# Optimization experiments

Hardware: AMD Instinct MI355X
Metric: run time of the kernel (lower is better)

Reference implementation:

```python
import jax, jax.numpy as jnp
import numpy as np

B, P, Q, D = 16, 4096, 1024, 256


def setup_inputs() -> dict:
    key = jax.random.key(0)
    k1, k2, k3, k4 = jax.random.split(key, 4)
    return {
        "passage_encodes": jax.random.normal(k1, (B, P, D), dtype=jnp.float32),
        "question_encodes": jax.random.normal(k2, (B, Q, D), dtype=jnp.float32),
        "w_attn": jax.random.normal(k3, (2 * D, 1), dtype=jnp.float32) * (1.0 / np.sqrt(2 * D)),
        "b_attn": jnp.zeros((1,), dtype=jnp.float32),
        "w_out": jax.random.normal(k4, (2 * D, 256), dtype=jnp.float32) * (1.0 / np.sqrt(2 * D)),
        "b_out": jnp.zeros((256,), dtype=jnp.float32),
    }


def reference(passage_encodes, question_encodes, w_attn, b_attn, w_out, b_out):
    # similarity matrix [B, P, Q]
    sim = jnp.einsum('bpd,bqd->bpq', passage_encodes, question_encodes)
    # context-to-question attention
    c2q = jax.nn.softmax(sim, axis=-1)                       # [B, P, Q]
    ctx2q = jnp.einsum('bpq,bqd->bpd', c2q, question_encodes)  # [B, P, D]
    # question-to-context attention (softmax over row-max)
    q2c = jax.nn.softmax(jnp.max(sim, axis=-1), axis=-1)     # [B, P]
    q2c_vec = jnp.einsum('bp,bpd->bd', q2c, passage_encodes)  # [B, D]
    tp = jnp.tanh(passage_encodes)
    concat = jnp.concatenate([
        tp * jnp.tanh(ctx2q),
        tp * jnp.tanh(q2c_vec)[:, None, :],  # broadcast instead of repeat
    ], axis=-1)                                              # [B, P, 2D]
    # attention reducer: linear -> softmax over sequence -> weighted sum
    w = jax.nn.softmax(jnp.einsum('bpc,co->bp', concat, w_attn) + b_attn[0], axis=1)
    reduced = jnp.einsum('bp,bpc->bc', w, concat)            # [B, 2D]
    return reduced @ w_out + b_out                            # [B, output_dim]
```

## Files before the change

kernel.cpp:

```cpp
#include <hip/hip_runtime.h>
#include <cmath>

#define BB 16
#define PP 4096
#define QQ 1024
#define DD 256

typedef __attribute__((ext_vector_type(8))) short short8;
typedef __attribute__((ext_vector_type(4))) float floatx4;
typedef __attribute__((ext_vector_type(4))) _Float16 half4;

static __device__ inline ushort bf16_rne(float x) {
  unsigned u = __float_as_uint(x);
  unsigned r = (u + 0x7fffu + ((u >> 16) & 1u)) >> 16;
  return (ushort)r;
}
static __device__ inline float bf16f(ushort h) { return __uint_as_float(((unsigned)h) << 16); }

static __device__ inline float ftanh(float x) {
  float e = __expf(2.0f * x);
  return 1.0f - 2.0f * __builtin_amdgcn_rcpf(e + 1.0f);
}

static __device__ inline void gl16(const void* g, void* l) {
  __builtin_amdgcn_global_load_lds(
      (const __attribute__((address_space(1))) unsigned int*)g,
      (__attribute__((address_space(3))) unsigned int*)l, 16, 0, 0);
}

__global__ __launch_bounds__(256) void kQprep(
    const float* __restrict__ ques, ushort* __restrict__ qb)
{
  const int b = blockIdx.y, qt = blockIdx.x;
  __shared__ float tile[32][260];
  const int tid = threadIdx.x;
  const float* src = ques + ((size_t)b * QQ + qt * 32) * DD;
  for (int i = tid; i < 32 * 64; i += 256) {
    int r = i >> 6, c = (i & 63) << 2;
    *(float4*)&tile[r][c] = *(const float4*)(src + r * DD + c);
  }
  ushort* blob = qb + (size_t)(b * 32 + qt) * 24576;
  {
    int r = tid >> 3;
    int j0 = (tid & 7) * 4;
    const float* rowp = src + r * DD + j0 * 8;
    float xs[32];
#pragma unroll
    for (int q4 = 0; q4 < 8; ++q4)
      *(float4*)&xs[q4 * 4] = *(const float4*)(rowp + q4 * 4);
#pragma unroll
    for (int jj = 0; jj < 4; ++jj) {
      int j = j0 + jj;
      ushort h8[8], l8[8];
#pragma unroll
      for (int e = 0; e < 8; ++e) {
        float x = xs[jj * 8 + e];
        ushort h = bf16_rne(x);
        h8[e] = h; l8[e] = bf16_rne(x - bf16f(h));
      }
      int g = r * 32 + (j ^ (r & 7));
      *(uint4*)&blob[(size_t)g * 8] = *(uint4*)h8;
      *(uint4*)&blob[8192 + (size_t)g * 8] = *(uint4*)l8;
    }
  }
  __syncthreads();
  {
    int d = tid;
    int s = (d >> 1) & 3;
    ushort h32[32];
#pragma unroll
    for (int r = 0; r < 32; ++r) h32[r] = bf16_rne(tile[r][d]);
#pragma unroll
    for (int k = 0; k < 4; ++k) {
      ushort g8[8];
#pragma unroll
      for (int e = 0; e < 4; ++e) {
        g8[e]     = h32[k * 4 + e];
        g8[4 + e] = h32[16 + k * 4 + e];
      }
      *(uint4*)&blob[16384 + (size_t)d * 32 + (k ^ s) * 8] = *(uint4*)g8;
    }
  }
}

__global__ __launch_bounds__(512, 1) void kA(
    const float* __restrict__ pass, const ushort* __restrict__ qb,
    const float* __restrict__ w_attn,
    _Float16* __restrict__ first_h, _Float16* __restrict__ tp_h,
    float* __restrict__ logit1,
    float* __restrict__ numpart, float* __restrict__ denpart)
{
  __shared__ alignas(16) char sm[147456];

  const int b    = blockIdx.y;
  const int p0   = blockIdx.x * 128;
  const int tid  = threadIdx.x;
  const int w    = tid >> 6;
  const int lane = tid & 63;
  const int l15  = lane & 15;
  const int quad = lane >> 4;
  const int swz  = l15 & 7;

  short8 bhi[8], blo[8];
  {
    const float* prow = pass + (((size_t)b * PP + p0 + w * 16 + l15) * DD);
#pragma unroll
    for (int c = 0; c < 8; ++c) {
      const float* p8 = prow + c * 32 + quad * 8;
      float4 x0 = *(const float4*)p8;
      float4 x1 = *(const float4*)(p8 + 4);
      float xs[8] = {x0.x, x0.y, x0.z, x0.w, x1.x, x1.y, x1.z, x1.w};
#pragma unroll
      for (int j = 0; j < 8; ++j) {
        ushort h = bf16_rne(xs[j]);
        ushort lo = bf16_rne(xs[j] - bf16f(h));
        bhi[c][j] = (short)h;
        blo[c][j] = (short)lo;
      }
    }
  }

  int goff[8];
#pragma unroll
  for (int c = 0; c < 8; ++c) goff[c] = (l15 * 32 + ((4 * c + quad) ^ swz)) * 8;
  const int vtoff = l15 * 32 + ((quad ^ ((l15 >> 1) & 3)) * 8);

  const ushort* tb = qb + (size_t)b * 32 * 24576;
  const int dma_l = w * 3072 + lane * 8;
  const int dma_s = w * 6144 + lane * 16;

  floatx4 accO[16];
#pragma unroll
  for (int i = 0; i < 16; ++i) accO[i] = (floatx4){0.f, 0.f, 0.f, 0.f};
  float mx = -INFINITY, ps = 0.f;
  short8 phi = {0, 0, 0, 0, 0, 0, 0, 0}, plo = {0, 0, 0, 0, 0, 0, 0, 0};

  {
    const ushort* gs = tb + dma_l;
    char* ld = sm + dma_s;
#pragma unroll
    for (int i = 0; i < 6; ++i) gl16(gs + i * 512, ld + i * 1024);
  }
  __syncthreads();

  for (int t = 0; t < 32; ++t) {
    const int ic = t % 3, ip = (t + 2) % 3, inx = (t + 1) % 3;
    char* cur = sm + ic * 49152;
    char* prv = sm + ip * 49152;
    if (t < 31) {
      const ushort* gs = tb + (size_t)(t + 1) * 24576 + dma_l;
      char* ld = sm + inx * 49152 + dma_s;
#pragma unroll
      for (int i = 0; i < 6; ++i) gl16(gs + i * 512, ld + i * 1024);
    }

    const ushort* Qhi = (const ushort*)cur;
    const ushort* Qlo = (const ushort*)(cur + 16384);
    floatx4 s0 = (floatx4){0.f, 0.f, 0.f, 0.f};
    floatx4 s1 = (floatx4){0.f, 0.f, 0.f, 0.f};
#pragma unroll
    for (int c = 0; c < 8; ++c) {
      short8 a0h = *(const short8*)&Qhi[goff[c]];
      short8 a0l = *(const short8*)&Qlo[goff[c]];
      short8 a1h = *(const short8*)&Qhi[goff[c] + 4096];
      short8 a1l = *(const short8*)&Qlo[goff[c] + 4096];
      s0 = __builtin_amdgcn_mfma_f32_16x16x32_bf16(a0h, bhi[c], s0, 0, 0, 0);
      s0 = __builtin_amdgcn_mfma_f32_16x16x32_bf16(a0h, blo[c], s0, 0, 0, 0);
      s0 = __builtin_amdgcn_mfma_f32_16x16x32_bf16(a0l, bhi[c], s0, 0, 0, 0);
      s1 = __builtin_amdgcn_mfma_f32_16x16x32_bf16(a1h, bhi[c], s1, 0, 0, 0);
      s1 = __builtin_amdgcn_mfma_f32_16x16x32_bf16(a1h, blo[c], s1, 0, 0, 0);
      s1 = __builtin_amdgcn_mfma_f32_16x16x32_bf16(a1l, bhi[c], s1, 0, 0, 0);
    }

    if (t > 0) {
      const ushort* TQ = (const ushort*)(prv + 32768);
#pragma unroll
      for (int nt = 0; nt < 16; ++nt) {
        short8 vhi = *(const short8*)&TQ[nt * 512 + vtoff];
        accO[nt] = __builtin_amdgcn_mfma_f32_16x16x32_bf16(phi, vhi, accO[nt], 0, 0, 0);
        accO[nt] = __builtin_amdgcn_mfma_f32_16x16x32_bf16(plo, vhi, accO[nt], 0, 0, 0);
      }
    }

    {
      short8 nph, npl;
#pragma unroll
      for (int r = 0; r < 4; ++r) {
        float s = s0[r];
        mx = fmaxf(mx, s);
        float x = __expf(s - 60.f);
        ps += x;
        ushort h = bf16_rne(x);
        nph[r] = (short)h;
        npl[r] = (short)bf16_rne(x - bf16f(h));
      }
#pragma unroll
      for (int r = 0; r < 4; ++r) {
        float s = s1[r];
        mx = fmaxf(mx, s);
        float x = __expf(s - 60.f);
        ps += x;
        ushort h = bf16_rne(x);
        nph[4 + r] = (short)h;
        npl[4 + r] = (short)bf16_rne(x - bf16f(h));
      }
      phi = nph;
      plo = npl;
    }
    __syncthreads();
  }

  {
    const ushort* TQ = (const ushort*)(sm + 49152 + 32768);
#pragma unroll
    for (int nt = 0; nt < 16; ++nt) {
      short8 vhi = *(const short8*)&TQ[nt * 512 + vtoff];
      accO[nt] = __builtin_amdgcn_mfma_f32_16x16x32_bf16(phi, vhi, accO[nt], 0, 0, 0);
      accO[nt] = __builtin_amdgcn_mfma_f32_16x16x32_bf16(plo, vhi, accO[nt], 0, 0, 0);
    }
  }

  ps += __shfl_xor(ps, 16);
  ps += __shfl_xor(ps, 32);
  mx = fmaxf(mx, __shfl_xor(mx, 16));
  mx = fmaxf(mx, __shfl_xor(mx, 32));

  __syncthreads();
  float* Of = (float*)(sm + w * 16640);
#pragma unroll
  for (int nt = 0; nt < 16; ++nt)
#pragma unroll
    for (int r = 0; r < 4; ++r)
      Of[(quad * 4 + r) * 260 + nt * 16 + l15] = accO[nt][r];
  const float4 w1 = *(const float4*)(w_attn + lane * 4);
  const size_t rowoff = (size_t)b * PP + p0 + w * 16;
  float4 qacc = make_float4(0.f, 0.f, 0.f, 0.f);
  float dacc = 0.f;
#pragma unroll
  for (int j = 0; j < 16; ++j) {
    float4 o = *(const float4*)&Of[j * 260 + lane * 4];
    float linv = 1.f / __shfl(ps, j);
    float4 pv4 = *(const float4*)(pass + (rowoff + j) * DD + lane * 4);
    float wj = __expf(__shfl(mx, j) - 60.f);
    qacc.x += wj * pv4.x; qacc.y += wj * pv4.y;
    qacc.z += wj * pv4.z; qacc.w += wj * pv4.w;
    dacc += wj;
    float tpx = ftanh(pv4.x), tpy = ftanh(pv4.y), tpz = ftanh(pv4.z), tpw = ftanh(pv4.w);
    float4 f;
    f.x = tpx * ftanh(o.x * linv);
    f.y = tpy * ftanh(o.y * linv);
    f.z = tpz * ftanh(o.z * linv);
    f.w = tpw * ftanh(o.w * linv);
    half4 fh = {(_Float16)f.x, (_Float16)f.y, (_Float16)f.z, (_Float16)f.w};
    half4 th = {(_Float16)tpx, (_Float16)tpy, (_Float16)tpz, (_Float16)tpw};
    *(half4*)(first_h + (rowoff + j) * DD + lane * 4) = fh;
    *(half4*)(tp_h + (rowoff + j) * DD + lane * 4) = th;
    float part = f.x * w1.x + f.y * w1.y + f.z * w1.z + f.w * w1.w;
    part += __shfl_xor(part, 1);  part += __shfl_xor(part, 2);
    part += __shfl_xor(part, 4);  part += __shfl_xor(part, 8);
    part += __shfl_xor(part, 16); part += __shfl_xor(part, 32);
    if (lane == 0) logit1[rowoff + j] = part;
  }

  float* redw = (float*)(sm + w * 16640);
  *(float4*)&redw[lane * 4] = qacc;
  if (lane == 0) redw[256] = dacc;
  __syncthreads();
  if (w == 0) {
    float4 s = make_float4(0.f, 0.f, 0.f, 0.f);
    float dsum = 0.f;
#pragma unroll
    for (int wv = 0; wv < 8; ++wv) {
      const float* rp = (const float*)(sm + wv * 16640);
      float4 v = *(const float4*)&rp[lane * 4];
      s.x += v.x; s.y += v.y; s.z += v.z; s.w += v.w;
      dsum += rp[256];
    }
    *(float4*)(numpart + (size_t)(blockIdx.x * 16 + b) * DD + lane * 4) = s;
    if (lane == 0) denpart[blockIdx.x * 16 + b] = dsum;
  }
}

__global__ __launch_bounds__(256) void kE(
    const _Float16* __restrict__ tp_h, const _Float16* __restrict__ first_h,
    const float* __restrict__ logit1,
    const float* __restrict__ numpart, const float* __restrict__ denpart,
    const float* __restrict__ w_attn,
    float* __restrict__ r1part, float* __restrict__ r2part, float* __restrict__ den2part)
{
  const int b = blockIdx.y, chunk = blockIdx.x;
  const int tid = threadIdx.x, r = tid >> 6, ln = tid & 63;
  __shared__ float s1[4][64][4];
  __shared__ float s2[4][64][4];
  __shared__ float sd[4][64];
  __shared__ alignas(16) float w2s[256];
  {
    float num = 0.f, den = 0.f;
#pragma unroll
    for (int c = 0; c < 32; ++c) {
      num += numpart[(size_t)(c * 16 + b) * DD + tid];
      den += denpart[c * 16 + b];
    }
    w2s[tid] = w_attn[DD + tid] * ftanh(num / den);
  }
  __syncthreads();
  const float4 wv = *(const float4*)&w2s[ln << 2];
  const float* lg = logit1 + (size_t)b * PP + chunk * 64;
  const size_t base = ((size_t)b * PP + chunk * 64) * DD;
  float a1[4] = {0.f, 0.f, 0.f, 0.f}, a2[4] = {0.f, 0.f, 0.f, 0.f};
  float den = 0.f;
  for (int p = r; p < 64; p += 4) {
    half4 f = *(const half4*)(first_h + base + (size_t)p * DD + ln * 4);
    half4 t = *(const half4*)(tp_h + base + (size_t)p * DD + ln * 4);
    float part = (float)t.x * wv.x + (float)t.y * wv.y +
                 (float)t.z * wv.z + (float)t.w * wv.w;
    part += __shfl_xor(part, 1);  part += __shfl_xor(part, 2);
    part += __shfl_xor(part, 4);  part += __shfl_xor(part, 8);
    part += __shfl_xor(part, 16); part += __shfl_xor(part, 32);
    float wgt = __expf(lg[p] + part);
    a1[0] += wgt * (float)f.x; a1[1] += wgt * (float)f.y;
    a1[2] += wgt * (float)f.z; a1[3] += wgt * (float)f.w;
    a2[0] += wgt * (float)t.x; a2[1] += wgt * (float)t.y;
    a2[2] += wgt * (float)t.z; a2[3] += wgt * (float)t.w;
    den += wgt;
  }
  *(float4*)&s1[r][ln][0] = *(float4*)a1;
  *(float4*)&s2[r][ln][0] = *(float4*)a2;
  sd[r][ln] = den;
  __syncthreads();
  if (r == 0) {
    float o1[4], o2[4];
#pragma unroll
    for (int i = 0; i < 4; ++i) {
      o1[i] = s1[0][ln][i] + s1[1][ln][i] + s1[2][ln][i] + s1[3][ln][i];
      o2[i] = s2[0][ln][i] + s2[1][ln][i] + s2[2][ln][i] + s2[3][ln][i];
    }
    *(float4*)(r1part + (size_t)(chunk * 16 + b) * DD + ln * 4) = *(float4*)o1;
    *(float4*)(r2part + (size_t)(chunk * 16 + b) * DD + ln * 4) = *(float4*)o2;
    if (ln == 0)
      den2part[chunk * 16 + b] = sd[0][0] + sd[1][0] + sd[2][0] + sd[3][0];
  }
}

__global__ __launch_bounds__(256) void kF(
    const float* __restrict__ r1part, const float* __restrict__ r2part,
    const float* __restrict__ den2part,
    const float* __restrict__ numpart, const float* __restrict__ denpart,
    const float* __restrict__ w_out, const float* __restrict__ b_out,
    float* __restrict__ out)
{
  const int b = blockIdx.x >> 2, og = blockIdx.x & 3;
  const int tid = threadIdx.x;
  __shared__ alignas(16) float R1[256], R2[256];
  __shared__ float sacc[4][64];
  {
    float red1 = 0.f, red2 = 0.f, den2 = 0.f;
#pragma unroll
    for (int c = 0; c < 64; ++c) {
      red1 += r1part[(size_t)(c * 16 + b) * DD + tid];
      red2 += r2part[(size_t)(c * 16 + b) * DD + tid];
      den2 += den2part[c * 16 + b];
    }
    float num = 0.f, den = 0.f;
#pragma unroll
    for (int c = 0; c < 32; ++c) {
      num += numpart[(size_t)(c * 16 + b) * DD + tid];
      den += denpart[c * 16 + b];
    }
    float t = ftanh(num / den);
    float inv = 1.f / den2;
    R1[tid] = red1 * inv;
    R2[tid] = red2 * inv * t;
  }
  __syncthreads();
  const int oi = tid & 63, ks = tid >> 6;
  const int o = og * 64 + oi;
  float acc = 0.f;
  for (int k = ks * 64; k < ks * 64 + 64; ++k) {
    acc += R1[k] * w_out[k * 256 + o];
    acc += R2[k] * w_out[(DD + k) * 256 + o];
  }
  sacc[ks][oi] = acc;
  __syncthreads();
  if (ks == 0) {
    float v = sacc[0][oi] + sacc[1][oi] + sacc[2][oi] + sacc[3][oi];
    out[b * 256 + o] = v + b_out[o];
  }
}

extern "C" void kernel_launch(void* const* d_in, const int* in_sizes, int n_in,
                              void* d_out, int out_size, void* d_ws, size_t ws_size,
                              hipStream_t stream) {
  const float* pass   = (const float*)d_in[0];
  const float* ques   = (const float*)d_in[1];
  const float* w_attn = (const float*)d_in[2];
  const float* w_out  = (const float*)d_in[4];
  const float* b_out  = (const float*)d_in[5];
  float* out = (float*)d_out;

  float* ws       = (float*)d_ws;
  float* logit1   = ws;
  float* numpart  = logit1   + (size_t)BB * PP;
  float* denpart  = numpart  + (size_t)32 * BB * DD;
  float* r1part   = denpart  + 32 * BB;
  float* r2part   = r1part   + (size_t)64 * BB * DD;
  float* den2part = r2part   + (size_t)64 * BB * DD;
  ushort* qbb     = (ushort*)(den2part + 64 * BB);
  _Float16* first_h = (_Float16*)(qbb + (size_t)BB * 32 * 24576);
  _Float16* tp_h    = first_h + (size_t)BB * PP * DD;

  kQprep<<<dim3(QQ / 32, BB), 256, 0, stream>>>(ques, qbb);
  kA    <<<dim3(PP / 128, BB), 512, 0, stream>>>(pass, qbb, w_attn,
                                                 first_h, tp_h, logit1,
                                                 numpart, denpart);
  kE    <<<dim3(64, BB), 256, 0, stream>>>(tp_h, first_h, logit1,
                                           numpart, denpart, w_attn,
                                           r1part, r2part, den2part);
  kF    <<<64, 256, 0, stream>>>(r1part, r2part, den2part,
                                 numpart, denpart, w_out, b_out, out);
}
```

Baseline: 323.8 us.

## Double kA block to 1024 threads covering 256 passage rows per block

The main attention kernel now runs 16 waves per block over 256 passage rows, so each staged question tile in shared memory serves twice as many rows, and each wave issues half as many async copies. The epilogue is split into two phases that reuse the shared buffer, with per-row softmax stats passed through shared memory. Downstream kernels reduce over 16 partials instead of 32. The grid halves to 256 blocks, which may underfill the GPU's CUs, and register pressure at 1024 threads could force spills.

```diff
diff --git a/kernel.cpp b/kernel.cpp
--- a/kernel.cpp
+++ b/kernel.cpp
@@ -83,7 +83,7 @@
   }
 }
 
-__global__ __launch_bounds__(512, 1) void kA(
+__global__ __launch_bounds__(1024, 1) void kA(
     const float* __restrict__ pass, const ushort* __restrict__ qb,
     const float* __restrict__ w_attn,
     _Float16* __restrict__ first_h, _Float16* __restrict__ tp_h,
@@ -93,7 +93,7 @@
   __shared__ alignas(16) char sm[147456];
 
   const int b    = blockIdx.y;
-  const int p0   = blockIdx.x * 128;
+  const int p0   = blockIdx.x * 256;
   const int tid  = threadIdx.x;
   const int w    = tid >> 6;
   const int lane = tid & 63;
@@ -126,8 +126,8 @@
   const int vtoff = l15 * 32 + ((quad ^ ((l15 >> 1) & 3)) * 8);
 
   const ushort* tb = qb + (size_t)b * 32 * 24576;
-  const int dma_l = w * 3072 + lane * 8;
-  const int dma_s = w * 6144 + lane * 16;
+  const int dma_l = w * 1536 + lane * 8;
+  const int dma_s = w * 3072 + lane * 16;
 
   floatx4 accO[16];
 #pragma unroll
@@ -139,7 +139,7 @@
     const ushort* gs = tb + dma_l;
     char* ld = sm + dma_s;
 #pragma unroll
-    for (int i = 0; i < 6; ++i) gl16(gs + i * 512, ld + i * 1024);
+    for (int i = 0; i < 3; ++i) gl16(gs + i * 512, ld + i * 1024);
   }
   __syncthreads();
 
@@ -151,7 +151,7 @@
       const ushort* gs = tb + (size_t)(t + 1) * 24576 + dma_l;
       char* ld = sm + inx * 49152 + dma_s;
 #pragma unroll
-      for (int i = 0; i < 6; ++i) gl16(gs + i * 512, ld + i * 1024);
+      for (int i = 0; i < 3; ++i) gl16(gs + i * 512, ld + i * 1024);
     }
 
     const ushort* Qhi = (const ushort*)cur;
@@ -224,45 +224,60 @@
   ps += __shfl_xor(ps, 32);
   mx = fmaxf(mx, __shfl_xor(mx, 16));
   mx = fmaxf(mx, __shfl_xor(mx, 32));
-
-  __syncthreads();
-  float* Of = (float*)(sm + w * 16640);
-#pragma unroll
-  for (int nt = 0; nt < 16; ++nt)
-#pragma unroll
-    for (int r = 0; r < 4; ++r)
-      Of[(quad * 4 + r) * 260 + nt * 16 + l15] = accO[nt][r];
+  float* psb = (float*)(sm + 135168);
+  float* mxb = (float*)(sm + 136192);
+  if (lane < 16) {
+    psb[w * 16 + l15] = ps;
+    mxb[w * 16 + l15] = mx;
+  }
+
   const float4 w1 = *(const float4*)(w_attn + lane * 4);
-  const size_t rowoff = (size_t)b * PP + p0 + w * 16;
   float4 qacc = make_float4(0.f, 0.f, 0.f, 0.f);
   float dacc = 0.f;
-#pragma unroll
-  for (int j = 0; j < 16; ++j) {
-    float4 o = *(const float4*)&Of[j * 260 + lane * 4];
-    float linv = 1.f / __shfl(ps, j);
-    float4 pv4 = *(const float4*)(pass + (rowoff + j) * DD + lane * 4);
-    float wj = __expf(__shfl(mx, j) - 60.f);
-    qacc.x += wj * pv4.x; qacc.y += wj * pv4.y;
-    qacc.z += wj * pv4.z; qacc.w += wj * pv4.w;
-    dacc += wj;
-    float tpx = ftanh(pv4.x), tpy = ftanh(pv4.y), tpz = ftanh(pv4.z), tpw = ftanh(pv4.w);
-    float4 f;
-    f.x = tpx * ftanh(o.x * linv);
-    f.y = tpy * ftanh(o.y * linv);
-    f.z = tpz * ftanh(o.z * linv);
-    f.w = tpw * ftanh(o.w * linv);
-    half4 fh = {(_Float16)f.x, (_Float16)f.y, (_Float16)f.z, (_Float16)f.w};
-    half4 th = {(_Float16)tpx, (_Float16)tpy, (_Float16)tpz, (_Float16)tpw};
-    *(half4*)(first_h + (rowoff + j) * DD + lane * 4) = fh;
-    *(half4*)(tp_h + (rowoff + j) * DD + lane * 4) = th;
-    float part = f.x * w1.x + f.y * w1.y + f.z * w1.z + f.w * w1.w;
-    part += __shfl_xor(part, 1);  part += __shfl_xor(part, 2);
-    part += __shfl_xor(part, 4);  part += __shfl_xor(part, 8);
-    part += __shfl_xor(part, 16); part += __shfl_xor(part, 32);
-    if (lane == 0) logit1[rowoff + j] = part;
-  }
-
-  float* redw = (float*)(sm + w * 16640);
+  for (int ph = 0; ph < 2; ++ph) {
+    __syncthreads();
+    if ((w >> 3) == ph) {
+      float* Of = (float*)(sm + (w & 7) * 16640);
+#pragma unroll
+      for (int nt = 0; nt < 16; ++nt)
+#pragma unroll
+        for (int r = 0; r < 4; ++r)
+          Of[(quad * 4 + r) * 260 + nt * 16 + l15] = accO[nt][r];
+    }
+    __syncthreads();
+#pragma unroll
+    for (int j = 0; j < 8; ++j) {
+      const int rl = w * 8 + j;
+      const int gr = ph * 128 + rl;
+      const float* ofp = (const float*)(sm + (rl >> 4) * 16640) + (rl & 15) * 260;
+      float4 o = *(const float4*)&ofp[lane * 4];
+      float linv = 1.f / psb[gr];
+      float wj = __expf(mxb[gr] - 60.f);
+      const size_t grow = (size_t)b * PP + p0 + gr;
+      float4 pv4 = *(const float4*)(pass + grow * DD + lane * 4);
+      qacc.x += wj * pv4.x; qacc.y += wj * pv4.y;
+      qacc.z += wj * pv4.z; qacc.w += wj * pv4.w;
+      dacc += wj;
+      float tpx = ftanh(pv4.x), tpy = ftanh(pv4.y), tpz = ftanh(pv4.z), tpw = ftanh(pv4.w);
+      float4 f;
+      f.x = tpx * ftanh(o.x * linv);
+      f.y = tpy * ftanh(o.y * linv);
+      f.z = tpz * ftanh(o.z * linv);
+      f.w = tpw * ftanh(o.w * linv);
+      half4 fh = {(_Float16)f.x, (_Float16)f.y, (_Float16)f.z, (_Float16)f.w};
+      half4 th = {(_Float16)tpx, (_Float16)tpy, (_Float16)tpz, (_Float16)tpw};
+      *(half4*)(first_h + grow * DD + lane * 4) = fh;
+      *(half4*)(tp_h + grow * DD + lane * 4) = th;
+      float part = f.x * w1.x + f.y * w1.y + f.z * w1.z + f.w * w1.w;
+      part += __shfl_xor(part, 1);  part += __shfl_xor(part, 2);
+      part += __shfl_xor(part, 4);  part += __shfl_xor(part, 8);
+      part += __shfl_xor(part, 16); part += __shfl_xor(part, 32);
+      if (lane == 0) logit1[grow] = part;
+    }
+  }
+
+  __syncthreads();
+  float* redw = (float*)sm + w * 260;
   *(float4*)&redw[lane * 4] = qacc;
   if (lane == 0) redw[256] = dacc;
   __syncthreads();
@@ -270,8 +285,8 @@
     float4 s = make_float4(0.f, 0.f, 0.f, 0.f);
     float dsum = 0.f;
 #pragma unroll
-    for (int wv = 0; wv < 8; ++wv) {
-      const float* rp = (const float*)(sm + wv * 16640);
+    for (int wv = 0; wv < 16; ++wv) {
+      const float* rp = (const float*)sm + wv * 260;
       float4 v = *(const float4*)&rp[lane * 4];
       s.x += v.x; s.y += v.y; s.z += v.z; s.w += v.w;
       dsum += rp[256];
@@ -297,7 +312,7 @@
   {
     float num = 0.f, den = 0.f;
 #pragma unroll
-    for (int c = 0; c < 32; ++c) {
+    for (int c = 0; c < 16; ++c) {
       num += numpart[(size_t)(c * 16 + b) * DD + tid];
       den += denpart[c * 16 + b];
     }
@@ -363,7 +378,7 @@
     }
     float num = 0.f, den = 0.f;
 #pragma unroll
-    for (int c = 0; c < 32; ++c) {
+    for (int c = 0; c < 16; ++c) {
       num += numpart[(size_t)(c * 16 + b) * DD + tid];
       den += denpart[c * 16 + b];
     }
@@ -410,9 +425,9 @@
   _Float16* tp_h    = first_h + (size_t)BB * PP * DD;
 
   kQprep<<<dim3(QQ / 32, BB), 256, 0, stream>>>(ques, qbb);
-  kA    <<<dim3(PP / 128, BB), 512, 0, stream>>>(pass, qbb, w_attn,
-                                                 first_h, tp_h, logit1,
-                                                 numpart, denpart);
+  kA    <<<dim3(PP / 256, BB), 1024, 0, stream>>>(pass, qbb, w_attn,
+                                                  first_h, tp_h, logit1,
+                                                  numpart, denpart);
   kE    <<<dim3(64, BB), 256, 0, stream>>>(tp_h, first_h, logit1,
                                            numpart, denpart, w_attn,
                                            r1part, r2part, den2part);
```

Measured after the change: 509.2 us. 1.57x slower.
